# Optimization experiments

Hardware: AMD Instinct MI355X
Metric: run time of the kernel (lower is better)

## Reference

```python
import jax, jax.numpy as jnp
import numpy as np

N_NODES = 100000
N_EDGES = 800000
N_GRAPHS = 128
D_IN = 84          # num_features_xd
D_HID = 840        # num_features_xd * 10
D_FC1 = 1024
D_OUT = 384


def setup_inputs() -> dict:
    key = jax.random.key(0)
    ks = jax.random.split(key, 12)
    x = jax.random.normal(ks[0], (N_NODES, D_IN), jnp.float32)
    edge_index = jax.random.randint(ks[1], (2, N_EDGES), 0, N_NODES)
    batch = jnp.sort(jax.random.randint(ks[2], (N_NODES,), 0, N_GRAPHS))

    def lin(k, fan_in, fan_out):
        bound = 1.0 / np.sqrt(fan_in)
        kw, kb = jax.random.split(k)
        W = jax.random.uniform(kw, (fan_in, fan_out), jnp.float32, -bound, bound)
        b = jax.random.uniform(kb, (fan_out,), jnp.float32, -bound, bound)
        return W, b

    W1, b1 = lin(ks[3], D_IN, D_IN)       # conv1.nn: Linear(84, 84)
    W2, b2 = lin(ks[4], D_IN, D_HID)      # conv2.nn: Linear(84, 840)
    Wg1, bg1 = lin(ks[5], 2 * D_HID, D_FC1)  # fc_g[0]: Linear(1680, 1024)
    Wg2, bg2 = lin(ks[6], D_FC1, D_OUT)      # fc_g[3]: Linear(1024, 384)
    return {"x": x, "edge_index": edge_index, "batch": batch,
            "W1": W1, "b1": b1, "W2": W2, "b2": b2,
            "Wg1": Wg1, "bg1": bg1, "Wg2": Wg2, "bg2": bg2}


def gin_conv(h, src, dst, W, b):
    # GINConv with eps=0: nn(x + sum_{j in N(i)} x_j), scatter-add over edges
    agg = jax.ops.segment_sum(h[src], dst, num_segments=N_NODES)
    return (h + agg) @ W + b


def reference(x, edge_index, batch, W1, b1, W2, b2, Wg1, bg1, Wg2, bg2):
    src, dst = edge_index[0], edge_index[1]
    h = jax.nn.relu(gin_conv(x, src, dst, W1, b1))    # [N, 84]
    h = jax.nn.relu(gin_conv(h, src, dst, W2, b2))    # [N, 840]

    # global max pool + global mean pool per graph
    counts = jax.ops.segment_sum(jnp.ones((N_NODES, 1), h.dtype), batch,
                                 num_segments=N_GRAPHS)          # [G, 1]
    sums = jax.ops.segment_sum(h, batch, num_segments=N_GRAPHS)  # [G, 840]
    meanp = sums / jnp.maximum(counts, 1.0)
    maxp = jax.ops.segment_max(h, batch, num_segments=N_GRAPHS)
    maxp = jnp.where(counts > 0, maxp, 0.0)

    z = jnp.concatenate([maxp, meanp], axis=1)        # [G, 1680]
    z = jax.nn.relu(z @ Wg1 + bg1)                    # dropout is identity in eval
    z = z @ Wg2 + bg2                                 # [G, 384]
    return z
```

## Files before the change

kernel.cpp:

```cpp
#include <hip/hip_runtime.h>

#define N_NODES 100000
#define N_EDGESC 800000
#define NGRAPH 128
#define DIN 84
#define DHID 840
#define DF1 1024
#define DOUTC 384
#define PBLK3 1563
#define KP1 1696
#define NBUCK 391
#define EPB 2048
#define XSTR 96

#define XBF_B 9375
#define W2T_B 336
#define W1T_B 36
#define CNT_B 49
#define G1_B  1696
#define G2_B  384
#define PREP_B (XBF_B + W2T_B + W1T_B + CNT_B + G1_B + G2_B)

typedef __attribute__((ext_vector_type(4))) float f32x4;
typedef __attribute__((ext_vector_type(8))) short bf16x8;

__device__ __forceinline__ unsigned short f2bf(float f) {
  union { float f; unsigned int u; } v; v.f = f;
  unsigned int r = v.u + 0x7FFFu + ((v.u >> 16) & 1u);
  return (unsigned short)(r >> 16);
}
__device__ __forceinline__ float bf2f(unsigned short h) {
  union { unsigned int u; float f; } v; v.u = ((unsigned int)h) << 16;
  return v.f;
}
__device__ __forceinline__ f32x4 bfq(uint2 p) {
  f32x4 r;
  r.x = bf2f((unsigned short)(p.x & 0xffff)); r.y = bf2f((unsigned short)(p.x >> 16));
  r.z = bf2f((unsigned short)(p.y & 0xffff)); r.w = bf2f((unsigned short)(p.y >> 16));
  return r;
}

__global__ __launch_bounds__(256) void k_bhist(const int* __restrict__ dst, int* __restrict__ bcnt) {
  __shared__ int h[NBUCK];
  int t = threadIdx.x;
  for (int i = t; i < NBUCK; i += 256) h[i] = 0;
  __syncthreads();
  int base = blockIdx.x * EPB;
  int e1 = min(base + EPB, N_EDGESC);
  for (int e = base + t; e < e1; e += 256)
    atomicAdd(&h[dst[e] >> 8], 1);
  __syncthreads();
  for (int i = t; i < NBUCK; i += 256) if (h[i]) atomicAdd(&bcnt[i], h[i]);
}

__global__ __launch_bounds__(512) void k_bscan(const int* __restrict__ bcnt, int* __restrict__ boff,
                                               int* __restrict__ bcur) {
  __shared__ int sd[512];
  int t = threadIdx.x;
  int v = (t < NBUCK) ? bcnt[t] : 0;
  sd[t] = v; __syncthreads();
  for (int off = 1; off < 512; off <<= 1) {
    int add = (t >= off) ? sd[t - off] : 0;
    __syncthreads();
    sd[t] += add;
    __syncthreads();
  }
  if (t <= NBUCK) {
    boff[t] = sd[t] - v;
    if (t < NBUCK) bcur[t] = sd[t] - v;
  }
}

__global__ __launch_bounds__(256) void k_bfill(const int* __restrict__ src, const int* __restrict__ dst,
                                               int* __restrict__ bcur, unsigned int* __restrict__ rec) {
  __shared__ int hcnt[NBUCK];
  __shared__ int hbase[NBUCK];
  int t = threadIdx.x;
  int e0 = blockIdx.x * EPB;
  int e1 = min(e0 + EPB, N_EDGESC);
  for (int i = t; i < NBUCK; i += 256) hcnt[i] = 0;
  __syncthreads();
  for (int e = e0 + t; e < e1; e += 256)
    atomicAdd(&hcnt[dst[e] >> 8], 1);
  __syncthreads();
  for (int i = t; i < NBUCK; i += 256) {
    int c = hcnt[i];
    hbase[i] = c ? atomicAdd(&bcur[i], c) : 0;
  }
  __syncthreads();
  for (int i = t; i < NBUCK; i += 256) hcnt[i] = 0;
  __syncthreads();
  for (int e = e0 + t; e < e1; e += 256) {
    int d = dst[e];
    int b = d >> 8;
    int r = atomicAdd(&hcnt[b], 1);
    rec[hbase[b] + r] = ((unsigned int)(d & 255) << 24) | (unsigned int)src[e];
  }
}

__global__ __launch_bounds__(256) void k_bsort(const unsigned int* __restrict__ rec, const int* __restrict__ boff,
                                               int* __restrict__ rowptr, int* __restrict__ csr) {
  __shared__ int lcnt[256];
  __shared__ int lcur[256];
  int b = blockIdx.x, t = threadIdx.x;
  int e0 = boff[b], e1 = boff[b + 1];
  lcnt[t] = 0;
  __syncthreads();
  for (int i = e0 + t; i < e1; i += 256) atomicAdd(&lcnt[rec[i] >> 24], 1);
  __syncthreads();
  int v = lcnt[t];
  for (int off = 1; off < 256; off <<= 1) {
    int add = (t >= off) ? lcnt[t - off] : 0;
    __syncthreads();
    lcnt[t] += add;
    __syncthreads();
  }
  int excl = lcnt[t] - v;
  int node = b * 256 + t;
  if (node < N_NODES) rowptr[node] = e0 + excl;
  lcur[t] = e0 + excl;
  if (b == NBUCK - 1 && t == 0) rowptr[N_NODES] = N_EDGESC;
  __syncthreads();
  for (int i = e0 + t; i < e1; i += 256) {
    unsigned int r = rec[i];
    int d = r >> 24;
    int pos = atomicAdd(&lcur[d], 1);
    csr[pos] = (int)(r & 0xFFFFFFu);
  }
}

__global__ __launch_bounds__(256) void k_prep(const float* __restrict__ x, unsigned short* __restrict__ xb,
                                              const float* __restrict__ W2, unsigned short* __restrict__ w2t,
                                              const float* __restrict__ W1, unsigned short* __restrict__ w1h,
                                              unsigned short* __restrict__ w1l,
                                              const int* __restrict__ batch, int* __restrict__ cnt,
                                              const float* __restrict__ Wg1, unsigned short* __restrict__ g1h,
                                              unsigned short* __restrict__ g1l,
                                              const float* __restrict__ Wg2, unsigned short* __restrict__ g2h,
                                              unsigned short* __restrict__ g2l) {
  __shared__ float tile[32][33];
  __shared__ int h[NGRAPH];
  int b = blockIdx.x, t = threadIdx.x;

  if (b < XBF_B) {
    int idx = b * 256 + t;
    if (idx >= N_NODES * 24) return;
    int r = idx / 24, c = idx - r * 24;
    uint2 p = {0u, 0u};
    if (c < 21) {
      f32x4 v = *(const f32x4*)&x[r * DIN + c * 4];
      p.x = (unsigned int)f2bf(v.x) | ((unsigned int)f2bf(v.y) << 16);
      p.y = (unsigned int)f2bf(v.z) | ((unsigned int)f2bf(v.w) << 16);
    }
    *(uint2*)&xb[r * XSTR + c * 4] = p;
    return;
  }
  b -= XBF_B;
  if (b < W2T_B) {
    int idx = b * 256 + t;
    if (idx >= 896 * 96) return;
    int n = idx / 96, k = idx % 96;
    float v = (n < DHID && k < DIN) ? W2[k * DHID + n] : 0.f;
    w2t[idx] = f2bf(v);
    return;
  }
  b -= W2T_B;
  if (b < W1T_B) {
    int idx = b * 256 + t;
    if (idx >= 96 * 96) return;
    int n = idx / 96, k = idx % 96;
    float v = (n < DIN && k < DIN) ? W1[k * DIN + n] : 0.f;
    unsigned short hh = f2bf(v);
    w1h[idx] = hh;
    w1l[idx] = f2bf(v - bf2f(hh));
    return;
  }
  b -= W1T_B;
  if (b < CNT_B) {
    if (t < NGRAPH) h[t] = 0;
    __syncthreads();
    int base = b * 2048;
    for (int j = 0; j < 8; j++) {
      int i = base + j * 256 + t;
      if (i < N_NODES) atomicAdd(&h[batch[i]], 1);
    }
    __syncthreads();
    if (t < NGRAPH && h[t] > 0) atomicAdd(&cnt[t], h[t]);
    return;
  }
  b -= CNT_B;
  const float* W; unsigned short *wh, *wl; int K, KPAD, N, vb;
  if (b < G1_B) { W = Wg1; wh = g1h; wl = g1l; K = 2 * DHID; KPAD = KP1; N = DF1; vb = b; }
  else          { W = Wg2; wh = g2h; wl = g2l; K = DF1; KPAD = DF1; N = DOUTC; vb = b - G1_B; }
  int kt = vb % (KPAD / 32), nt2 = vb / (KPAD / 32);
  int k0 = kt * 32, n0 = nt2 * 32;
  int r = t >> 3, c4 = (t & 7) * 4;
  int k = k0 + r;
  f32x4 v = {0.f, 0.f, 0.f, 0.f};
  if (k < K) v = *(const f32x4*)&W[(size_t)k * N + n0 + c4];
  tile[r][c4 + 0] = v.x; tile[r][c4 + 1] = v.y; tile[r][c4 + 2] = v.z; tile[r][c4 + 3] = v.w;
  __syncthreads();
  int n = t >> 3;
  float f0 = tile[c4 + 0][n], f1 = tile[c4 + 1][n], f2 = tile[c4 + 2][n], f3 = tile[c4 + 3][n];
  unsigned short h0 = f2bf(f0), h1_ = f2bf(f1), h2_ = f2bf(f2), h3_ = f2bf(f3);
  uint2 ph, pl;
  ph.x = (unsigned int)h0 | ((unsigned int)h1_ << 16);
  ph.y = (unsigned int)h2_ | ((unsigned int)h3_ << 16);
  pl.x = (unsigned int)f2bf(f0 - bf2f(h0)) | ((unsigned int)f2bf(f1 - bf2f(h1_)) << 16);
  pl.y = (unsigned int)f2bf(f2 - bf2f(h2_)) | ((unsigned int)f2bf(f3 - bf2f(h3_)) << 16);
  *(uint2*)&wh[(size_t)(n0 + n) * KPAD + k0 + c4] = ph;
  *(uint2*)&wl[(size_t)(n0 + n) * KPAD + k0 + c4] = pl;
}

__global__ __launch_bounds__(256) void k_agg1c(const unsigned short* __restrict__ xb,
                                               const int* __restrict__ rowptr,
                                               const int* __restrict__ csr,
                                               unsigned short* __restrict__ aggh) {
  int t = threadIdx.x;
  int wv = t >> 6, l = t & 63;
  int grp = (l >= 42) ? 2 : (l >= 21 ? 1 : 0);
  int li = l - grp * 21;
  int node = blockIdx.x * 12 + wv * 3 + grp;
  bool act = (li < 21) && (node < N_NODES);
  if (l == 63) {
    uint2 z = {0u, 0u};
    for (int g = 0; g < 3; g++) {
      int nd = blockIdx.x * 12 + wv * 3 + g;
      if (nd < N_NODES) {
        *(uint2*)&aggh[nd * XSTR + 84] = z; *(uint2*)&aggh[nd * XSTR + 88] = z; *(uint2*)&aggh[nd * XSTR + 92] = z;
      }
    }
  }
  int nclamp = min(node, N_NODES - 1);
  int r0 = rowptr[nclamp];
  int r1 = act ? rowptr[nclamp + 1] : r0;
  f32x4 a = {0.f, 0.f, 0.f, 0.f};
  if (act) a = bfq(*(const uint2*)&xb[nclamp * XSTR + li * 4]);
  int e = r0;
  for (; e + 8 <= r1; e += 8) {
    int s0 = csr[e], s1 = csr[e + 1], s2 = csr[e + 2], s3 = csr[e + 3];
    int s4 = csr[e + 4], s5 = csr[e + 5], s6 = csr[e + 6], s7 = csr[e + 7];
    uint2 q0 = *(const uint2*)&xb[s0 * XSTR + li * 4];
    uint2 q1 = *(const uint2*)&xb[s1 * XSTR + li * 4];
    uint2 q2 = *(const uint2*)&xb[s2 * XSTR + li * 4];
    uint2 q3 = *(const uint2*)&xb[s3 * XSTR + li * 4];
    uint2 q4 = *(const uint2*)&xb[s4 * XSTR + li * 4];
    uint2 q5 = *(const uint2*)&xb[s5 * XSTR + li * 4];
    uint2 q6 = *(const uint2*)&xb[s6 * XSTR + li * 4];
    uint2 q7 = *(const uint2*)&xb[s7 * XSTR + li * 4];
    a += ((bfq(q0) + bfq(q1)) + (bfq(q2) + bfq(q3))) + ((bfq(q4) + bfq(q5)) + (bfq(q6) + bfq(q7)));
  }
  for (; e + 4 <= r1; e += 4) {
    int s0 = csr[e], s1 = csr[e + 1], s2 = csr[e + 2], s3 = csr[e + 3];
    uint2 q0 = *(const uint2*)&xb[s0 * XSTR + li * 4];
    uint2 q1 = *(const uint2*)&xb[s1 * XSTR + li * 4];
    uint2 q2 = *(const uint2*)&xb[s2 * XSTR + li * 4];
    uint2 q3 = *(const uint2*)&xb[s3 * XSTR + li * 4];
    a += (bfq(q0) + bfq(q1)) + (bfq(q2) + bfq(q3));
  }
  for (; e < r1; e++) {
    int s = csr[e];
    a += bfq(*(const uint2*)&xb[s * XSTR + li * 4]);
  }
  if (act) {
    uint2 p;
    p.x = (unsigned int)f2bf(a.x) | ((unsigned int)f2bf(a.y) << 16);
    p.y = (unsigned int)f2bf(a.z) | ((unsigned int)f2bf(a.w) << 16);
    *(uint2*)&aggh[node * XSTR + li * 4] = p;
  }
}

__global__ __launch_bounds__(256) void k_conv1m2(const unsigned short* __restrict__ aggh,
                                                 const unsigned short* __restrict__ w1h,
                                                 const unsigned short* __restrict__ w1l,
                                                 const float* __restrict__ b1,
                                                 unsigned short* __restrict__ h1b) {
  int t = threadIdx.x;
  int m0 = blockIdx.x * 64;
  int wv = t >> 6, l = t & 63;
  int lr = l & 15, lk = (l >> 4) * 8;
  int row = m0 + wv * 16 + lr;
  bool inb = row < N_NODES;
  bf16x8 ah[3];
  #pragma unroll
  for (int kk = 0; kk < 3; kk++) {
    bf16x8 vh = {0, 0, 0, 0, 0, 0, 0, 0};
    if (inb) vh = *(const bf16x8*)&aggh[(size_t)row * XSTR + lk + kk * 32];
    ah[kk] = vh;
  }
  #pragma unroll
  for (int nt = 0; nt < 6; nt++) {
    f32x4 acc = {0.f, 0.f, 0.f, 0.f};
    #pragma unroll
    for (int kk = 0; kk < 3; kk++) {
      bf16x8 bh = *(const bf16x8*)&w1h[(nt * 16 + lr) * 96 + lk + kk * 32];
      bf16x8 bl = *(const bf16x8*)&w1l[(nt * 16 + lr) * 96 + lk + kk * 32];
      acc = __builtin_amdgcn_mfma_f32_16x16x32_bf16(ah[kk], bh, acc, 0, 0, 0);
      acc = __builtin_amdgcn_mfma_f32_16x16x32_bf16(ah[kk], bl, acc, 0, 0, 0);
    }
    int col = nt * 16 + lr;
    if (col < DIN) {
      float bias = b1[col];
      int rbase = m0 + wv * 16 + (l >> 4) * 4;
      #pragma unroll
      for (int j = 0; j < 4; j++) {
        if (rbase + j < N_NODES)
          h1b[(rbase + j) * XSTR + col] = f2bf(fmaxf(acc[j] + bias, 0.f));
      }
    }
  }
}

__global__ __launch_bounds__(256) void k_agg2(const unsigned short* __restrict__ h1b, const int* __restrict__ rowptr,
                                              const int* __restrict__ csr, unsigned short* __restrict__ out) {
  int t = threadIdx.x;
  int wv = t >> 6, l = t & 63;
  int grp = (l >= 42) ? 2 : (l >= 21 ? 1 : 0);
  int li = l - grp * 21;
  int node = blockIdx.x * 12 + wv * 3 + grp;
  bool act = (li < 21) && (node < N_NODES);
  int nclamp = min(node, N_NODES - 1);
  int r0 = rowptr[nclamp];
  int r1 = act ? rowptr[nclamp + 1] : r0;
  f32x4 a = {0.f, 0.f, 0.f, 0.f};
  if (act) a = bfq(*(const uint2*)&h1b[nclamp * XSTR + li * 4]);
  int e = r0;
  for (; e + 8 <= r1; e += 8) {
    int s0 = csr[e], s1 = csr[e + 1], s2 = csr[e + 2], s3 = csr[e + 3];
    int s4 = csr[e + 4], s5 = csr[e + 5], s6 = csr[e + 6], s7 = csr[e + 7];
    uint2 q0 = *(const uint2*)&h1b[s0 * XSTR + li * 4];
    uint2 q1 = *(const uint2*)&h1b[s1 * XSTR + li * 4];
    uint2 q2 = *(const uint2*)&h1b[s2 * XSTR + li * 4];
    uint2 q3 = *(const uint2*)&h1b[s3 * XSTR + li * 4];
    uint2 q4 = *(const uint2*)&h1b[s4 * XSTR + li * 4];
    uint2 q5 = *(const uint2*)&h1b[s5 * XSTR + li * 4];
    uint2 q6 = *(const uint2*)&h1b[s6 * XSTR + li * 4];
    uint2 q7 = *(const uint2*)&h1b[s7 * XSTR + li * 4];
    a += ((bfq(q0) + bfq(q1)) + (bfq(q2) + bfq(q3))) + ((bfq(q4) + bfq(q5)) + (bfq(q6) + bfq(q7)));
  }
  for (; e + 4 <= r1; e += 4) {
    int s0 = csr[e], s1 = csr[e + 1], s2 = csr[e + 2], s3 = csr[e + 3];
    uint2 q0 = *(const uint2*)&h1b[s0 * XSTR + li * 4];
    uint2 q1 = *(const uint2*)&h1b[s1 * XSTR + li * 4];
    uint2 q2 = *(const uint2*)&h1b[s2 * XSTR + li * 4];
    uint2 q3 = *(const uint2*)&h1b[s3 * XSTR + li * 4];
    a += (bfq(q0) + bfq(q1)) + (bfq(q2) + bfq(q3));
  }
  for (; e < r1; e++) {
    int s = csr[e];
    a += bfq(*(const uint2*)&h1b[s * XSTR + li * 4]);
  }
  if (act) {
    uint2 p;
    p.x = (unsigned int)f2bf(a.x) | ((unsigned int)f2bf(a.y) << 16);
    p.y = (unsigned int)f2bf(a.z) | ((unsigned int)f2bf(a.w) << 16);
    *(uint2*)&out[node * XSTR + li * 4] = p;
  }
}

__global__ __launch_bounds__(256) void k_conv2pool4(const unsigned short* __restrict__ aggb,
                                                    const unsigned short* __restrict__ w2t,
                                                    const float* __restrict__ b2,
                                                    const int* __restrict__ batch,
                                                    float2* __restrict__ pm, float2* __restrict__ pm1,
                                                    int* __restrict__ blkg,
                                                    int* __restrict__ maxb, float* __restrict__ sump) {
  constexpr int LDA = 104;
  __shared__ __align__(16) unsigned short At[64 * LDA];
  int t = threadIdx.x;
  int w = t >> 6, l = t & 63;
  int b = blockIdx.x >> 1;
  int half = blockIdx.x & 1;
  int m0 = b * 64;
  int lr = l & 15, hi = l >> 4, lk = hi * 8;

  for (int idx = t; idx < 64 * 12; idx += 256) {
    int r = idx / 12, c = idx - r * 12;
    uint4 v = {0u, 0u, 0u, 0u};
    int row = m0 + r;
    if (row < N_NODES) v = *(const uint4*)&aggb[row * XSTR + c * 8];
    *(uint4*)&At[r * LDA + c * 8] = v;
  }
  int g0 = batch[m0];
  int g1 = batch[min(m0 + 63, N_NODES - 1)];
  bool fast = (g0 == g1) && (m0 + 63 < N_NODES);
  __syncthreads();

  bf16x8 afr[4][3];
  #pragma unroll
  for (int rg = 0; rg < 4; rg++)
    #pragma unroll
    for (int kk = 0; kk < 3; kk++)
      afr[rg][kk] = *(bf16x8*)&At[(rg * 16 + lr) * LDA + lk + kk * 32];

  int pbase = half * 28 + w * 7;

  if (fast) {
    for (int i = 0; i < 7; i++) {
      int c = (pbase + i) * 16 + lr;
      const unsigned short* bp = &w2t[c * 96 + lk];
      bf16x8 b0v = *(const bf16x8*)(bp);
      bf16x8 b1v = *(const bf16x8*)(bp + 32);
      bf16x8 b2v = *(const bf16x8*)(bp + 64);
      float bias = (c < DHID) ? b2[c] : 0.f;
      float mx = 0.f, sm = 0.f;
      #pragma unroll
      for (int rg = 0; rg < 4; rg++) {
        f32x4 a_ = {0.f, 0.f, 0.f, 0.f};
        a_ = __builtin_amdgcn_mfma_f32_16x16x32_bf16(afr[rg][0], b0v, a_, 0, 0, 0);
        a_ = __builtin_amdgcn_mfma_f32_16x16x32_bf16(afr[rg][1], b1v, a_, 0, 0, 0);
        a_ = __builtin_amdgcn_mfma_f32_16x16x32_bf16(afr[rg][2], b2v, a_, 0, 0, 0);
        float v0 = fmaxf(a_[0] + bias, 0.f);
        float v1 = fmaxf(a_[1] + bias, 0.f);
        float v2 = fmaxf(a_[2] + bias, 0.f);
        float v3 = fmaxf(a_[3] + bias, 0.f);
        mx = fmaxf(mx, fmaxf(fmaxf(v0, v1), fmaxf(v2, v3)));
        sm += (v0 + v1) + (v2 + v3);
      }
      mx = fmaxf(mx, __shfl_xor(mx, 16)); sm += __shfl_xor(sm, 16);
      mx = fmaxf(mx, __shfl_xor(mx, 32)); sm += __shfl_xor(sm, 32);
      if (hi == 0 && c < DHID) pm[(size_t)b * DHID + c] = make_float2(mx, sm);
    }
  } else {
    int grow[4][4];
    #pragma unroll
    for (int rg = 0; rg < 4; rg++)
      #pragma unroll
      for (int j = 0; j < 4; j++) {
        int row = m0 + rg * 16 + hi * 4 + j;
        grow[rg][j] = (row < N_NODES) ? batch[row] : -1;
      }
    for (int i = 0; i < 7; i++) {
      int c = (pbase + i) * 16 + lr;
      const unsigned short* bp = &w2t[c * 96 + lk];
      bf16x8 b0v = *(const bf16x8*)(bp);
      bf16x8 b1v = *(const bf16x8*)(bp + 32);
      bf16x8 b2v = *(const bf16x8*)(bp + 64);
      float bias = (c < DHID) ? b2[c] : 0.f;
      float mx0 = 0.f, sm0 = 0.f, mx1 = 0.f, sm1 = 0.f;
      float vv[4][4];
      #pragma unroll
      for (int rg = 0; rg < 4; rg++) {
        f32x4 a_ = {0.f, 0.f, 0.f, 0.f};
        a_ = __builtin_amdgcn_mfma_f32_16x16x32_bf16(afr[rg][0], b0v, a_, 0, 0, 0);
        a_ = __builtin_amdgcn_mfma_f32_16x16x32_bf16(afr[rg][1], b1v, a_, 0, 0, 0);
        a_ = __builtin_amdgcn_mfma_f32_16x16x32_bf16(afr[rg][2], b2v, a_, 0, 0, 0);
        #pragma unroll
        for (int j = 0; j < 4; j++) {
          float v = fmaxf(a_[j] + bias, 0.f);
          vv[rg][j] = v;
          if (grow[rg][j] == g0) { mx0 = fmaxf(mx0, v); sm0 += v; }
          if (grow[rg][j] == g1) { mx1 = fmaxf(mx1, v); sm1 += v; }
        }
      }
      mx0 = fmaxf(mx0, __shfl_xor(mx0, 16)); sm0 += __shfl_xor(sm0, 16);
      mx0 = fmaxf(mx0, __shfl_xor(mx0, 32)); sm0 += __shfl_xor(sm0, 32);
      mx1 = fmaxf(mx1, __shfl_xor(mx1, 16)); sm1 += __shfl_xor(sm1, 16);
      mx1 = fmaxf(mx1, __shfl_xor(mx1, 32)); sm1 += __shfl_xor(sm1, 32);
      if (hi == 0 && c < DHID) {
        pm[(size_t)b * DHID + c] = make_float2(mx0, sm0);
        pm1[(size_t)b * DHID + c] = make_float2(mx1, sm1);
      }
      if (g1 - g0 >= 2) {
        for (int g = g0 + 1; g < g1; g++) {
          float mx = 0.f, sm = 0.f;
          #pragma unroll
          for (int rg = 0; rg < 4; rg++)
            #pragma unroll
            for (int j = 0; j < 4; j++)
              if (grow[rg][j] == g) { mx = fmaxf(mx, vv[rg][j]); sm += vv[rg][j]; }
          mx = fmaxf(mx, __shfl_xor(mx, 16)); sm += __shfl_xor(sm, 16);
          mx = fmaxf(mx, __shfl_xor(mx, 32)); sm += __shfl_xor(sm, 32);
          if (hi == 0 && c < DHID) {
            atomicMax(&maxb[g * DHID + c], __float_as_int(mx));
            atomicAdd(&sump[g * DHID + c], sm);
          }
        }
      }
    }
  }
  if (t == 0 && half == 0) { blkg[b * 2] = g0; blkg[b * 2 + 1] = g1; }
}

__global__ __launch_bounds__(256) void k_pool2(const float2* __restrict__ pm, const float2* __restrict__ pm1,
                                               const int* __restrict__ blkg, const int* __restrict__ cnt,
                                               const int* __restrict__ maxb, const float* __restrict__ sump,
                                               unsigned short* __restrict__ zh, unsigned short* __restrict__ zl) {
  __shared__ int sstart[NGRAPH];
  int g = blockIdx.x, t = threadIdx.x;
  if (t == 0) {
    int s = 0;
    for (int i = 0; i < NGRAPH; i++) { sstart[i] = s; s += cnt[i]; }
  }
  __syncthreads();
  int c0 = cnt[g];
  int ns = sstart[g], ne = ns + c0;
  int b0 = ns / 64, b1 = (c0 > 0) ? (ne - 1) / 64 : b0 - 1;
  for (int c = t; c < DHID; c += 256) {
    float mx = __int_as_float(maxb[g * DHID + c]);
    float sm = sump[g * DHID + c];
    for (int b = b0; b <= b1; b++) {
      int gg0 = blkg[2 * b], gg1 = blkg[2 * b + 1];
      if (gg0 == g)      { float2 p = pm[(size_t)b * DHID + c];  mx = fmaxf(mx, p.x); sm += p.y; }
      else if (gg1 == g) { float2 p = pm1[(size_t)b * DHID + c]; mx = fmaxf(mx, p.x); sm += p.y; }
    }
    float vmax = (c0 > 0) ? mx : 0.f;
    float vmean = sm / (float)max(c0, 1);
    unsigned short hm = f2bf(vmax);
    zh[g * KP1 + c] = hm;
    zl[g * KP1 + c] = f2bf(vmax - bf2f(hm));
    unsigned short he = f2bf(vmean);
    zh[g * KP1 + DHID + c] = he;
    zl[g * KP1 + DHID + c] = f2bf(vmean - bf2f(he));
  }
  if (t < KP1 - 2 * DHID) {
    zh[g * KP1 + 2 * DHID + t] = 0;
    zl[g * KP1 + 2 * DHID + t] = 0;
  }
}

__global__ __launch_bounds__(256) void k_mlp1m(const unsigned short* __restrict__ zh, const unsigned short* __restrict__ zl,
                                               const unsigned short* __restrict__ wh, const unsigned short* __restrict__ wl,
                                               const float* __restrict__ bg,
                                               unsigned short* __restrict__ z1h, unsigned short* __restrict__ z1l) {
  int t = threadIdx.x, w = t >> 6, l = t & 63;
  int lr = l & 15, hi = l >> 4, lk = hi * 8;
  int b = blockIdx.x;
  int n0 = (b >> 1) * 16;
  int m0 = (b & 1) * 64 + w * 16;
  const unsigned short* za = &zh[(size_t)(m0 + lr) * KP1 + lk];
  const unsigned short* zb = &zl[(size_t)(m0 + lr) * KP1 + lk];
  const unsigned short* wa = &wh[(size_t)(n0 + lr) * KP1 + lk];
  const unsigned short* wb = &wl[(size_t)(n0 + lr) * KP1 + lk];
  f32x4 acc = {0.f, 0.f, 0.f, 0.f};
  for (int ks = 0; ks < KP1 / 32; ks++) {
    bf16x8 ah = *(const bf16x8*)(za + ks * 32);
    bf16x8 al = *(const bf16x8*)(zb + ks * 32);
    bf16x8 bh = *(const bf16x8*)(wa + ks * 32);
    bf16x8 bl = *(const bf16x8*)(wb + ks * 32);
    acc = __builtin_amdgcn_mfma_f32_16x16x32_bf16(ah, bh, acc, 0, 0, 0);
    acc = __builtin_amdgcn_mfma_f32_16x16x32_bf16(al, bh, acc, 0, 0, 0);
    acc = __builtin_amdgcn_mfma_f32_16x16x32_bf16(ah, bl, acc, 0, 0, 0);
  }
  int col = n0 + lr;
  float bias = bg[col];
  #pragma unroll
  for (int j = 0; j < 4; j++) {
    int row = m0 + hi * 4 + j;
    float v = fmaxf(acc[j] + bias, 0.f);
    unsigned short h = f2bf(v);
    z1h[row * DF1 + col] = h;
    z1l[row * DF1 + col] = f2bf(v - bf2f(h));
  }
}

__global__ __launch_bounds__(256) void k_mlp2m(const unsigned short* __restrict__ z1h, const unsigned short* __restrict__ z1l,
                                               const unsigned short* __restrict__ wh, const unsigned short* __restrict__ wl,
                                               const float* __restrict__ bg, float* __restrict__ out) {
  int t = threadIdx.x, w = t >> 6, l = t & 63;
  int lr = l & 15, hi = l >> 4, lk = hi * 8;
  int b = blockIdx.x;
  int n0 = (b >> 1) * 16;
  int m0 = (b & 1) * 64 + w * 16;
  const unsigned short* za = &z1h[(size_t)(m0 + lr) * DF1 + lk];
  const unsigned short* zb = &z1l[(size_t)(m0 + lr) * DF1 + lk];
  const unsigned short* wa = &wh[(size_t)(n0 + lr) * DF1 + lk];
  const unsigned short* wb = &wl[(size_t)(n0 + lr) * DF1 + lk];
  f32x4 acc = {0.f, 0.f, 0.f, 0.f};
  for (int ks = 0; ks < DF1 / 32; ks++) {
    bf16x8 ah = *(const bf16x8*)(za + ks * 32);
    bf16x8 al = *(const bf16x8*)(zb + ks * 32);
    bf16x8 bh = *(const bf16x8*)(wa + ks * 32);
    bf16x8 bl = *(const bf16x8*)(wb + ks * 32);
    acc = __builtin_amdgcn_mfma_f32_16x16x32_bf16(ah, bh, acc, 0, 0, 0);
    acc = __builtin_amdgcn_mfma_f32_16x16x32_bf16(al, bh, acc, 0, 0, 0);
    acc = __builtin_amdgcn_mfma_f32_16x16x32_bf16(ah, bl, acc, 0, 0, 0);
  }
  int col = n0 + lr;
  float bias = bg[col];
  #pragma unroll
  for (int j = 0; j < 4; j++) {
    int row = m0 + hi * 4 + j;
    out[row * DOUTC + col] = acc[j] + bias;
  }
}

static constexpr size_t AL(size_t x) { return (x + 255) & ~(size_t)255; }

extern "C" void kernel_launch(void* const* d_in, const int* in_sizes, int n_in,
                              void* d_out, int out_size, void* d_ws, size_t ws_size,
                              hipStream_t stream) {
  const float* x   = (const float*)d_in[0];
  const int*  edge = (const int*)d_in[1];
  const int*  batch= (const int*)d_in[2];
  const float* W1  = (const float*)d_in[3];
  const float* b1  = (const float*)d_in[4];
  const float* W2  = (const float*)d_in[5];
  const float* b2  = (const float*)d_in[6];
  const float* Wg1 = (const float*)d_in[7];
  const float* bg1 = (const float*)d_in[8];
  const float* Wg2 = (const float*)d_in[9];
  const float* bg2 = (const float*)d_in[10];
  float* out = (float*)d_out;
  const int* src = edge;
  const int* dst = edge + N_EDGESC;

  size_t o = 0;
  size_t OFF_AGG = o;  o += AL((size_t)N_NODES * DIN * 4);
  size_t OFF_AGH = o;  o += AL((size_t)N_NODES * XSTR * 2);
  size_t OFF_H1  = o;  o += AL((size_t)N_NODES * XSTR * 2);
  size_t OFF_AGB = o;  o += AL((size_t)N_NODES * XSTR * 2);
  size_t OFF_CSR = o;  o += AL((size_t)N_EDGESC * 4);
  size_t OFF_REC = o;  o += AL((size_t)N_EDGESC * 4);
  size_t OFF_W2T = o;  o += AL((size_t)896 * 96 * 2);
  size_t OFF_W1H = o;  o += AL((size_t)96 * 96 * 2);
  size_t OFF_W1L = o;  o += AL((size_t)96 * 96 * 2);
  size_t OFF_G1H = o;  o += AL((size_t)DF1 * KP1 * 2);
  size_t OFF_G1L = o;  o += AL((size_t)DF1 * KP1 * 2);
  size_t OFF_G2H = o;  o += AL((size_t)DOUTC * DF1 * 2);
  size_t OFF_G2L = o;  o += AL((size_t)DOUTC * DF1 * 2);
  size_t OFF_ZH  = o;  o += AL((size_t)NGRAPH * KP1 * 2);
  size_t OFF_ZL  = o;  o += AL((size_t)NGRAPH * KP1 * 2);
  size_t OFF_Z1H = o;  o += AL((size_t)NGRAPH * DF1 * 2);
  size_t OFF_Z1L = o;  o += AL((size_t)NGRAPH * DF1 * 2);
  size_t OFF_RP  = o;  o += AL((size_t)(N_NODES + 1) * 4);
  size_t OFF_BOF = o;  o += AL((NBUCK + 1) * 4);
  size_t OFF_BCU = o;  o += AL(NBUCK * 4);
  size_t OFF_BC  = o;  o += AL(NBUCK * 4);
  size_t OFF_MAX = o;  o += AL((size_t)NGRAPH * DHID * 4);
  size_t OFF_SUM = o;  o += AL((size_t)NGRAPH * DHID * 4);
  size_t OFF_CNT = o;  o += AL(NGRAPH * 4);
  size_t TOTAL = o;
  size_t ZERO0 = OFF_BC, ZEROB = TOTAL - OFF_BC;
  if (ws_size < TOTAL) return;

  size_t PB = AL((size_t)PBLK3 * DHID * 8);
  size_t OFF_PM  = OFF_AGG;
  size_t OFF_PM1 = OFF_AGG + PB;
  size_t OFF_BLG = OFF_AGG + 2 * PB;

  char* ws = (char*)d_ws;
  unsigned short* aggh = (unsigned short*)(ws + OFF_AGH);
  unsigned short* h1b = (unsigned short*)(ws + OFF_H1);
  unsigned short* aggb = (unsigned short*)(ws + OFF_AGB);
  unsigned short* xb   = (unsigned short*)(ws + OFF_AGB);
  int* csr   = (int*)(ws + OFF_CSR);
  unsigned int* rec = (unsigned int*)(ws + OFF_REC);
  unsigned short* w2t = (unsigned short*)(ws + OFF_W2T);
  unsigned short* w1h = (unsigned short*)(ws + OFF_W1H);
  unsigned short* w1l = (unsigned short*)(ws + OFF_W1L);
  unsigned short* g1h = (unsigned short*)(ws + OFF_G1H);
  unsigned short* g1l = (unsigned short*)(ws + OFF_G1L);
  unsigned short* g2h = (unsigned short*)(ws + OFF_G2H);
  unsigned short* g2l = (unsigned short*)(ws + OFF_G2L);
  unsigned short* zh  = (unsigned short*)(ws + OFF_ZH);
  unsigned short* zl  = (unsigned short*)(ws + OFF_ZL);
  unsigned short* z1h = (unsigned short*)(ws + OFF_Z1H);
  unsigned short* z1l = (unsigned short*)(ws + OFF_Z1L);
  int* rowptr = (int*)(ws + OFF_RP);
  int* boff  = (int*)(ws + OFF_BOF);
  int* bcur  = (int*)(ws + OFF_BCU);
  int* bcnt  = (int*)(ws + OFF_BC);
  int* maxb  = (int*)(ws + OFF_MAX);
  float* sump= (float*)(ws + OFF_SUM);
  int* cnt   = (int*)(ws + OFF_CNT);
  float2* pm  = (float2*)(ws + OFF_PM);
  float2* pm1 = (float2*)(ws + OFF_PM1);
  int* blkg  = (int*)(ws + OFF_BLG);

  hipMemsetAsync(ws + ZERO0, 0, ZEROB, stream);

  k_prep<<<PREP_B, 256, 0, stream>>>(x, xb, W2, w2t, W1, w1h, w1l, batch, cnt,
                                     Wg1, g1h, g1l, Wg2, g2h, g2l);

  int nbb = (N_EDGESC + EPB - 1) / EPB;
  k_bhist<<<nbb, 256, 0, stream>>>(dst, bcnt);
  k_bscan<<<1, 512, 0, stream>>>(bcnt, boff, bcur);
  k_bfill<<<nbb, 256, 0, stream>>>(src, dst, bcur, rec);
  k_bsort<<<NBUCK, 256, 0, stream>>>(rec, boff, rowptr, csr);

  k_agg1c<<<(N_NODES + 11) / 12, 256, 0, stream>>>(xb, rowptr, csr, aggh);
  k_conv1m2<<<PBLK3, 256, 0, stream>>>(aggh, w1h, w1l, b1, h1b);
  k_agg2<<<(N_NODES + 11) / 12, 256, 0, stream>>>(h1b, rowptr, csr, aggb);
  k_conv2pool4<<<2 * PBLK3, 256, 0, stream>>>(aggb, w2t, b2, batch, pm, pm1, blkg, maxb, sump);
  k_pool2<<<NGRAPH, 256, 0, stream>>>(pm, pm1, blkg, cnt, maxb, sump, zh, zl);

  k_mlp1m<<<(DF1 / 16) * 2, 256, 0, stream>>>(zh, zl, g1h, g1l, bg1, z1h, z1l);
  k_mlp2m<<<(DOUTC / 16) * 2, 256, 0, stream>>>(z1h, z1l, g2h, g2l, bg2, out);
}
```

Before: 247.2 us.

## Fuse edge histogram into prep kernel and precompute per-block bucket offsets

The per-block dst bucket histogram is folded into the existing k_prep launch, and each block's counts are stored in a block-by-bucket matrix. A new column-scan kernel turns that matrix into per-block bucket base offsets. The fill kernel then scatters without recounting or issuing global atomics on bucket cursors. This removes two kernel launches and a redundant histogram pass, at the cost of an extra scan kernel and a strided hrow matrix read/write.

```diff
diff --git a/kernel.cpp b/kernel.cpp
--- a/kernel.cpp
+++ b/kernel.cpp
@@ -11,15 +11,17 @@
 #define KP1 1696
 #define NBUCK 391
 #define EPB 2048
+#define EBLK 391
 #define XSTR 96
 
+#define BH_B  EBLK
 #define XBF_B 9375
 #define W2T_B 336
 #define W1T_B 36
 #define CNT_B 49
 #define G1_B  1696
 #define G2_B  384
-#define PREP_B (XBF_B + W2T_B + W1T_B + CNT_B + G1_B + G2_B)
+#define PREP_B (BH_B + XBF_B + W2T_B + W1T_B + CNT_B + G1_B + G2_B)
 
 typedef __attribute__((ext_vector_type(4))) float f32x4;
 typedef __attribute__((ext_vector_type(8))) short bf16x8;
@@ -40,96 +42,9 @@
   return r;
 }
 
-__global__ __launch_bounds__(256) void k_bhist(const int* __restrict__ dst, int* __restrict__ bcnt) {
-  __shared__ int h[NBUCK];
-  int t = threadIdx.x;
-  for (int i = t; i < NBUCK; i += 256) h[i] = 0;
-  __syncthreads();
-  int base = blockIdx.x * EPB;
-  int e1 = min(base + EPB, N_EDGESC);
-  for (int e = base + t; e < e1; e += 256)
-    atomicAdd(&h[dst[e] >> 8], 1);
-  __syncthreads();
-  for (int i = t; i < NBUCK; i += 256) if (h[i]) atomicAdd(&bcnt[i], h[i]);
-}
-
-__global__ __launch_bounds__(512) void k_bscan(const int* __restrict__ bcnt, int* __restrict__ boff,
-                                               int* __restrict__ bcur) {
-  __shared__ int sd[512];
-  int t = threadIdx.x;
-  int v = (t < NBUCK) ? bcnt[t] : 0;
-  sd[t] = v; __syncthreads();
-  for (int off = 1; off < 512; off <<= 1) {
-    int add = (t >= off) ? sd[t - off] : 0;
-    __syncthreads();
-    sd[t] += add;
-    __syncthreads();
-  }
-  if (t <= NBUCK) {
-    boff[t] = sd[t] - v;
-    if (t < NBUCK) bcur[t] = sd[t] - v;
-  }
-}
-
-__global__ __launch_bounds__(256) void k_bfill(const int* __restrict__ src, const int* __restrict__ dst,
-                                               int* __restrict__ bcur, unsigned int* __restrict__ rec) {
-  __shared__ int hcnt[NBUCK];
-  __shared__ int hbase[NBUCK];
-  int t = threadIdx.x;
-  int e0 = blockIdx.x * EPB;
-  int e1 = min(e0 + EPB, N_EDGESC);
-  for (int i = t; i < NBUCK; i += 256) hcnt[i] = 0;
-  __syncthreads();
-  for (int e = e0 + t; e < e1; e += 256)
-    atomicAdd(&hcnt[dst[e] >> 8], 1);
-  __syncthreads();
-  for (int i = t; i < NBUCK; i += 256) {
-    int c = hcnt[i];
-    hbase[i] = c ? atomicAdd(&bcur[i], c) : 0;
-  }
-  __syncthreads();
-  for (int i = t; i < NBUCK; i += 256) hcnt[i] = 0;
-  __syncthreads();
-  for (int e = e0 + t; e < e1; e += 256) {
-    int d = dst[e];
-    int b = d >> 8;
-    int r = atomicAdd(&hcnt[b], 1);
-    rec[hbase[b] + r] = ((unsigned int)(d & 255) << 24) | (unsigned int)src[e];
-  }
-}
-
-__global__ __launch_bounds__(256) void k_bsort(const unsigned int* __restrict__ rec, const int* __restrict__ boff,
-                                               int* __restrict__ rowptr, int* __restrict__ csr) {
-  __shared__ int lcnt[256];
-  __shared__ int lcur[256];
-  int b = blockIdx.x, t = threadIdx.x;
-  int e0 = boff[b], e1 = boff[b + 1];
-  lcnt[t] = 0;
-  __syncthreads();
-  for (int i = e0 + t; i < e1; i += 256) atomicAdd(&lcnt[rec[i] >> 24], 1);
-  __syncthreads();
-  int v = lcnt[t];
-  for (int off = 1; off < 256; off <<= 1) {
-    int add = (t >= off) ? lcnt[t - off] : 0;
-    __syncthreads();
-    lcnt[t] += add;
-    __syncthreads();
-  }
-  int excl = lcnt[t] - v;
-  int node = b * 256 + t;
-  if (node < N_NODES) rowptr[node] = e0 + excl;
-  lcur[t] = e0 + excl;
-  if (b == NBUCK - 1 && t == 0) rowptr[N_NODES] = N_EDGESC;
-  __syncthreads();
-  for (int i = e0 + t; i < e1; i += 256) {
-    unsigned int r = rec[i];
-    int d = r >> 24;
-    int pos = atomicAdd(&lcur[d], 1);
-    csr[pos] = (int)(r & 0xFFFFFFu);
-  }
-}
-
-__global__ __launch_bounds__(256) void k_prep(const float* __restrict__ x, unsigned short* __restrict__ xb,
+__global__ __launch_bounds__(256) void k_prep(const int* __restrict__ dst, int* __restrict__ hrow,
+                                              int* __restrict__ bcnt,
+                                              const float* __restrict__ x, unsigned short* __restrict__ xb,
                                               const float* __restrict__ W2, unsigned short* __restrict__ w2t,
                                               const float* __restrict__ W1, unsigned short* __restrict__ w1h,
                                               unsigned short* __restrict__ w1l,
@@ -140,8 +55,23 @@
                                               unsigned short* __restrict__ g2l) {
   __shared__ float tile[32][33];
   __shared__ int h[NGRAPH];
+  __shared__ int hb[NBUCK];
   int b = blockIdx.x, t = threadIdx.x;
 
+  if (b < BH_B) {
+    for (int i = t; i < NBUCK; i += 256) hb[i] = 0;
+    __syncthreads();
+    int e0 = b * EPB, e1 = min(e0 + EPB, N_EDGESC);
+    for (int e = e0 + t; e < e1; e += 256) atomicAdd(&hb[dst[e] >> 8], 1);
+    __syncthreads();
+    for (int i = t; i < NBUCK; i += 256) {
+      int c = hb[i];
+      hrow[b * NBUCK + i] = c;
+      if (c) atomicAdd(&bcnt[i], c);
+    }
+    return;
+  }
+  b -= BH_B;
   if (b < XBF_B) {
     int idx = b * 256 + t;
     if (idx >= N_NODES * 24) return;
@@ -210,6 +140,79 @@
   pl.y = (unsigned int)f2bf(f2 - bf2f(h2_)) | ((unsigned int)f2bf(f3 - bf2f(h3_)) << 16);
   *(uint2*)&wh[(size_t)(n0 + n) * KPAD + k0 + c4] = ph;
   *(uint2*)&wl[(size_t)(n0 + n) * KPAD + k0 + c4] = pl;
+}
+
+__global__ __launch_bounds__(512) void k_bcolscan(const int* __restrict__ bcnt, int* __restrict__ hrow,
+                                                  int* __restrict__ boff) {
+  __shared__ int sr[512];
+  __shared__ int sd[512];
+  int g = blockIdx.x, t = threadIdx.x;
+  sr[t] = (t < g) ? bcnt[t] : 0;
+  __syncthreads();
+  for (int off = 256; off > 0; off >>= 1) {
+    if (t < off) sr[t] += sr[t + off];
+    __syncthreads();
+  }
+  int base0 = sr[0];
+  if (t == 0) boff[g] = base0;
+  if (g == 0 && t == 0) boff[NBUCK] = N_EDGESC;
+  int v = (t < EBLK) ? hrow[t * NBUCK + g] : 0;
+  sd[t] = v;
+  __syncthreads();
+  for (int off = 1; off < 512; off <<= 1) {
+    int add = (t >= off) ? sd[t - off] : 0;
+    __syncthreads();
+    sd[t] += add;
+    __syncthreads();
+  }
+  if (t < EBLK) hrow[t * NBUCK + g] = base0 + sd[t] - v;
+}
+
+__global__ __launch_bounds__(256) void k_bfill2(const int* __restrict__ src, const int* __restrict__ dst,
+                                                const int* __restrict__ hrow, unsigned int* __restrict__ rec) {
+  __shared__ int hcnt[NBUCK];
+  __shared__ int hbase[NBUCK];
+  int t = threadIdx.x, b = blockIdx.x;
+  for (int i = t; i < NBUCK; i += 256) { hcnt[i] = 0; hbase[i] = hrow[b * NBUCK + i]; }
+  __syncthreads();
+  int e0 = b * EPB, e1 = min(e0 + EPB, N_EDGESC);
+  for (int e = e0 + t; e < e1; e += 256) {
+    int d = dst[e];
+    int bk = d >> 8;
+    int r = atomicAdd(&hcnt[bk], 1);
+    rec[hbase[bk] + r] = ((unsigned int)(d & 255) << 24) | (unsigned int)src[e];
+  }
+}
+
+__global__ __launch_bounds__(256) void k_bsort(const unsigned int* __restrict__ rec, const int* __restrict__ boff,
+                                               int* __restrict__ rowptr, int* __restrict__ csr) {
+  __shared__ int lcnt[256];
+  __shared__ int lcur[256];
+  int b = blockIdx.x, t = threadIdx.x;
+  int e0 = boff[b], e1 = boff[b + 1];
+  lcnt[t] = 0;
+  __syncthreads();
+  for (int i = e0 + t; i < e1; i += 256) atomicAdd(&lcnt[rec[i] >> 24], 1);
+  __syncthreads();
+  int v = lcnt[t];
+  for (int off = 1; off < 256; off <<= 1) {
+    int add = (t >= off) ? lcnt[t - off] : 0;
+    __syncthreads();
+    lcnt[t] += add;
+    __syncthreads();
+  }
+  int excl = lcnt[t] - v;
+  int node = b * 256 + t;
+  if (node < N_NODES) rowptr[node] = e0 + excl;
+  lcur[t] = e0 + excl;
+  if (b == NBUCK - 1 && t == 0) rowptr[N_NODES] = N_EDGESC;
+  __syncthreads();
+  for (int i = e0 + t; i < e1; i += 256) {
+    unsigned int r = rec[i];
+    int d = r >> 24;
+    int pos = atomicAdd(&lcur[d], 1);
+    csr[pos] = (int)(r & 0xFFFFFFu);
+  }
 }
 
 __global__ __launch_bounds__(256) void k_agg1c(const unsigned short* __restrict__ xb,
@@ -612,6 +615,7 @@
   size_t OFF_AGB = o;  o += AL((size_t)N_NODES * XSTR * 2);
   size_t OFF_CSR = o;  o += AL((size_t)N_EDGESC * 4);
   size_t OFF_REC = o;  o += AL((size_t)N_EDGESC * 4);
+  size_t OFF_HRW = o;  o += AL((size_t)EBLK * NBUCK * 4);
   size_t OFF_W2T = o;  o += AL((size_t)896 * 96 * 2);
   size_t OFF_W1H = o;  o += AL((size_t)96 * 96 * 2);
   size_t OFF_W1L = o;  o += AL((size_t)96 * 96 * 2);
@@ -625,7 +629,6 @@
   size_t OFF_Z1L = o;  o += AL((size_t)NGRAPH * DF1 * 2);
   size_t OFF_RP  = o;  o += AL((size_t)(N_NODES + 1) * 4);
   size_t OFF_BOF = o;  o += AL((NBUCK + 1) * 4);
-  size_t OFF_BCU = o;  o += AL(NBUCK * 4);
   size_t OFF_BC  = o;  o += AL(NBUCK * 4);
   size_t OFF_MAX = o;  o += AL((size_t)NGRAPH * DHID * 4);
   size_t OFF_SUM = o;  o += AL((size_t)NGRAPH * DHID * 4);
@@ -646,6 +649,7 @@
   unsigned short* xb   = (unsigned short*)(ws + OFF_AGB);
   int* csr   = (int*)(ws + OFF_CSR);
   unsigned int* rec = (unsigned int*)(ws + OFF_REC);
+  int* hrow  = (int*)(ws + OFF_HRW);
   unsigned short* w2t = (unsigned short*)(ws + OFF_W2T);
   unsigned short* w1h = (unsigned short*)(ws + OFF_W1H);
   unsigned short* w1l = (unsigned short*)(ws + OFF_W1L);
@@ -659,7 +663,6 @@
   unsigned short* z1l = (unsigned short*)(ws + OFF_Z1L);
   int* rowptr = (int*)(ws + OFF_RP);
   int* boff  = (int*)(ws + OFF_BOF);
-  int* bcur  = (int*)(ws + OFF_BCU);
   int* bcnt  = (int*)(ws + OFF_BC);
   int* maxb  = (int*)(ws + OFF_MAX);
   float* sump= (float*)(ws + OFF_SUM);
@@ -670,13 +673,10 @@
 
   hipMemsetAsync(ws + ZERO0, 0, ZEROB, stream);
 
-  k_prep<<<PREP_B, 256, 0, stream>>>(x, xb, W2, w2t, W1, w1h, w1l, batch, cnt,
-                                     Wg1, g1h, g1l, Wg2, g2h, g2l);
-
-  int nbb = (N_EDGESC + EPB - 1) / EPB;
-  k_bhist<<<nbb, 256, 0, stream>>>(dst, bcnt);
-  k_bscan<<<1, 512, 0, stream>>>(bcnt, boff, bcur);
-  k_bfill<<<nbb, 256, 0, stream>>>(src, dst, bcur, rec);
+  k_prep<<<PREP_B, 256, 0, stream>>>(dst, hrow, bcnt, x, xb, W2, w2t, W1, w1h, w1l,
+                                     batch, cnt, Wg1, g1h, g1l, Wg2, g2h, g2l);
+  k_bcolscan<<<NBUCK, 512, 0, stream>>>(bcnt, hrow, boff);
+  k_bfill2<<<EBLK, 256, 0, stream>>>(src, dst, hrow, rec);
   k_bsort<<<NBUCK, 256, 0, stream>>>(rec, boff, rowptr, csr);
 
   k_agg1c<<<(N_NODES + 11) / 12, 256, 0, stream>>>(xb, rowptr, csr, aggh);
```

New measurement: 238.6 us. 1.04x faster.
